# Kernel optimization log

Measured on AMD Instinct MI355X. Metric: run time of the kernel, lower is better.

## Reference

```python
import jax, jax.numpy as jnp
import numpy as np

B, GH, GW = 64, 14, 14
H = 512   # features_len == lstm hidden size == lstm_len
E = 512   # embedding_len
A = 512   # attention_len
V = 10000 # wordmap_len
MAXCAP = 50


def setup_inputs() -> dict:
    key = jax.random.key(0)
    ks = jax.random.split(key, 12)
    s = 0.02
    caplens = jax.random.randint(ks[2], (B, 1), 2, MAXCAP + 1, jnp.int32)
    caplens = caplens.at[0, 0].set(MAXCAP)  # ensure max(decode_lengths) == MAXCAP-1 (static T)
    return dict(
        image_features=jax.random.normal(ks[0], (B, GH, GW, H), jnp.float32),
        caps=jax.random.randint(ks[1], (B, MAXCAP), 0, V, jnp.int32),
        caplens=caplens,
        emb_table=jax.random.normal(ks[3], (V, E), jnp.float32) * s,
        W_ih=jax.random.normal(ks[4], (4 * H, E + H), jnp.float32) * s,
        W_hh=jax.random.normal(ks[5], (4 * H, H), jnp.float32) * s,
        b_ih=jnp.zeros((4 * H,), jnp.float32),
        b_hh=jnp.zeros((4 * H,), jnp.float32),
        W_enc=jax.random.normal(ks[6], (A, H), jnp.float32) * s,
        b_enc=jnp.zeros((A,), jnp.float32),
        W_dec=jax.random.normal(ks[7], (A, H), jnp.float32) * s,
        b_dec=jnp.zeros((A,), jnp.float32),
        W_full=jax.random.normal(ks[8], (1, A), jnp.float32) * s,
        b_full=jnp.zeros((1,), jnp.float32),
        W_score=jax.random.normal(ks[9], (V, H), jnp.float32) * s,
        b_score=jnp.zeros((V,), jnp.float32),
    )


def _forward(image_features, emb_table, W_ih, W_hh, b_ih, b_hh,
             W_enc, b_enc, W_dec, b_dec, W_full, b_full, W_score, b_score,
             caps, caplens):
    Bsz = image_features.shape[0]
    feats = image_features.reshape(Bsz, -1, image_features.shape[-1])  # (B, P, H)
    cl = caplens[:, 0]
    sort_ind = jnp.argsort(-cl)                      # descending sort by caption length
    cl = cl[sort_ind]
    feats = feats[sort_ind]
    caps_s = caps[sort_ind]
    decode_lengths = cl - 1
    T = caps.shape[1] - 1                            # static; setup guarantees max(decode_lengths)==T
    emb = emb_table[caps_s]                          # (B, MAXCAP, E)
    enc_att = jnp.einsum('bph,ah->bpa', feats, W_enc) + b_enc  # precomputed encoder attention proj
    mask = jnp.arange(T)[None, :] < decode_lengths[:, None]    # (B, T): row active at step t

    h0 = jnp.zeros((Bsz, feats.shape[-1]), feats.dtype)
    c0 = jnp.zeros_like(h0)

    def step(carry, xs):
        h, c = carry
        emb_t, m_t = xs                              # (B,E), (B,)
        # attention (show-attend-tell style)
        att2 = h @ W_dec.T + b_dec                   # (B, A)
        e = jnp.einsum('bpa,a->bp', jax.nn.relu(enc_att + att2[:, None, :]), W_full[0]) + b_full[0]
        alpha = jax.nn.softmax(e, axis=-1)           # (B, P)
        ctx = jnp.einsum('bp,bph->bh', alpha, feats) # (B, H)
        # LSTMCell
        x = jnp.concatenate([emb_t, ctx], axis=1)    # (B, E+H)
        gates = x @ W_ih.T + b_ih + h @ W_hh.T + b_hh
        i, f, g, o = jnp.split(gates, 4, axis=1)
        c_new = jax.nn.sigmoid(f) * c + jax.nn.sigmoid(i) * jnp.tanh(g)
        h_new = jax.nn.sigmoid(o) * jnp.tanh(c_new)
        score = h_new @ W_score.T + b_score          # (B, V)
        m = m_t[:, None]
        # rows past their decode length keep stale state and write zeros (matches :k slicing)
        h = jnp.where(m, h_new, h)
        c = jnp.where(m, c_new, c)
        return (h, c), (jnp.where(m, score, jnp.zeros((), score.dtype)),
                        jnp.where(m, alpha, jnp.zeros((), alpha.dtype)))

    (_, _), (scores, weights) = jax.lax.scan(
        step, (h0, c0), (emb[:, :T, :].transpose(1, 0, 2), mask.T))
    scores = scores.transpose(1, 0, 2)   # (B, T, V)
    weights = weights.transpose(1, 0, 2) # (B, T, P)
    return scores, caps_s, decode_lengths, weights, sort_ind


def reference(image_features, caps, caplens, emb_table, W_ih, W_hh, b_ih, b_hh,
              W_enc, b_enc, W_dec, b_dec, W_full, b_full, W_score, b_score):
    return _forward(image_features, emb_table, W_ih, W_hh, b_ih, b_hh,
                    W_enc, b_enc, W_dec, b_dec, W_full, b_full, W_score, b_score,
                    caps, caplens)
```

## Files before the change

kernel.cpp:

```cpp
#include <hip/hip_runtime.h>
#include <math.h>


#define WS_SORT   0
#define WS_DL     64
#define WS_NB     128
#define WS_ROWOFF 192
#define WS_CAPS   256
#define WS_RMAP   3456
#define WS_H      6592
#define WS_C      39360
#define WS_ATT2   72128
#define WS_E      104896
#define WS_Z      117696
#define WS_CTXP   117952
#define WS_PG     249024
#define WS_HALL   2346176
#define WS_ENC    3951808

#define OUT_SCORES 0
#define OUT_CAPS   31360000
#define OUT_DL     31363200
#define OUT_W      31363264
#define OUT_SORT   31977920

#define KC  32
#define LST 68
#define LSW 196

__device__ __forceinline__ float sigm(float x) { return 1.f / (1.f + expf(-x)); }

__device__ __forceinline__ float4 f4add(float4 a, float4 b) {
  return make_float4(a.x + b.x, a.y + b.y, a.z + b.z, a.w + b.w);
}

__device__ __forceinline__ int swz128(int m) { return (m >> 3) * 12 + (m & 7); }

__device__ __forceinline__ void gemm_acc(const float* __restrict__ As, const float* __restrict__ Bs,
                                         float acc[8][8], int tx, int ty) {
#pragma unroll 8
  for (int kk = 0; kk < KC; ++kk) {
    const float4* ar = (const float4*)(As + kk * LST + tx * 8);
    const float4* br = (const float4*)(Bs + kk * LST + ty * 8);
    float4 a0 = ar[0], a1 = ar[1];
    float4 b0 = br[0], b1 = br[1];
    float av[8] = {a0.x, a0.y, a0.z, a0.w, a1.x, a1.y, a1.z, a1.w};
    float bv[8] = {b0.x, b0.y, b0.z, b0.w, b1.x, b1.y, b1.z, b1.w};
#pragma unroll
    for (int i = 0; i < 8; ++i)
#pragma unroll
      for (int j = 0; j < 8; ++j)
        acc[i][j] = fmaf(av[i], bv[j], acc[i][j]);
  }
}

__device__ __forceinline__ void load_tile_strided(const float* __restrict__ src, int row0, int ld, int k0,
                                                  float* __restrict__ dst, int tid, int nrows_valid) {
#pragma unroll
  for (int i = 0; i < 8; ++i) {
    int lin = tid + 64 * i;
    int m = lin >> 3, kf = lin & 7;
    float4 v = make_float4(0.f, 0.f, 0.f, 0.f);
    if (m < nrows_valid) v = *(const float4*)(src + (long)(row0 + m) * ld + k0 + kf * 4);
    dst[(kf * 4 + 0) * LST + m] = v.x;
    dst[(kf * 4 + 1) * LST + m] = v.y;
    dst[(kf * 4 + 2) * LST + m] = v.z;
    dst[(kf * 4 + 3) * LST + m] = v.w;
  }
}

__device__ __forceinline__ void load_tile_gather(const float* __restrict__ src, const int* __restrict__ bases,
                                                 int k0, float* __restrict__ dst, int tid) {
#pragma unroll
  for (int i = 0; i < 8; ++i) {
    int lin = tid + 64 * i;
    int m = lin >> 3, kf = lin & 7;
    float4 v = *(const float4*)(src + bases[m] + k0 + kf * 4);
    dst[(kf * 4 + 0) * LST + m] = v.x;
    dst[(kf * 4 + 1) * LST + m] = v.y;
    dst[(kf * 4 + 2) * LST + m] = v.z;
    dst[(kf * 4 + 3) * LST + m] = v.w;
  }
}

__device__ __forceinline__ void stage128_strided(const float* __restrict__ src, int row0, int ld, int k0,
                                                 float* __restrict__ dst, int tid, int nrows_valid) {
#pragma unroll
  for (int i = 0; i < 2; ++i) {
    int lin = tid + 256 * i;
    int m = lin >> 2, kf = lin & 3;
    float4 v = make_float4(0.f, 0.f, 0.f, 0.f);
    if (m < nrows_valid) v = *(const float4*)(src + (long)(row0 + m) * ld + k0 + kf * 4);
    int mc = swz128(m);
    dst[(kf * 4 + 0) * LSW + mc] = v.x;
    dst[(kf * 4 + 1) * LSW + mc] = v.y;
    dst[(kf * 4 + 2) * LSW + mc] = v.z;
    dst[(kf * 4 + 3) * LSW + mc] = v.w;
  }
}

__device__ __forceinline__ void stage128_gather(const float* __restrict__ src, const int* __restrict__ bases,
                                                int k0, float* __restrict__ dst, int tid) {
#pragma unroll
  for (int i = 0; i < 2; ++i) {
    int lin = tid + 256 * i;
    int m = lin >> 2, kf = lin & 3;
    float4 v = *(const float4*)(src + bases[m] + k0 + kf * 4);
    int mc = swz128(m);
    dst[(kf * 4 + 0) * LSW + mc] = v.x;
    dst[(kf * 4 + 1) * LSW + mc] = v.y;
    dst[(kf * 4 + 2) * LSW + mc] = v.z;
    dst[(kf * 4 + 3) * LSW + mc] = v.w;
  }
}

__device__ __forceinline__ void gemm_acc128(const float* __restrict__ As, const float* __restrict__ Bs,
                                            float acc[8][8], int tx, int ty) {
#pragma unroll
  for (int kk = 0; kk < 16; ++kk) {
    const float4* ar = (const float4*)(As + kk * LSW + tx * 12);
    const float4* br = (const float4*)(Bs + kk * LSW + ty * 12);
    float4 a0 = ar[0], a1 = ar[1];
    float4 b0 = br[0], b1 = br[1];
    float av[8] = {a0.x, a0.y, a0.z, a0.w, a1.x, a1.y, a1.z, a1.w};
    float bv[8] = {b0.x, b0.y, b0.z, b0.w, b1.x, b1.y, b1.z, b1.w};
#pragma unroll
    for (int i = 0; i < 8; ++i)
#pragma unroll
      for (int j = 0; j < 8; ++j)
        acc[i][j] = fmaf(av[i], bv[j], acc[i][j]);
  }
}

__global__ __launch_bounds__(64) void setup_kernel(const int* __restrict__ caps, const int* __restrict__ caplens,
                                                   float* __restrict__ ws, float* __restrict__ out) {
  __shared__ int cl_s[64], so_s[64], dl_s[64], nb_s[49], ro_s[50];
  int i = threadIdx.x;
  cl_s[i] = caplens[i];
  __syncthreads();
  int cli = cl_s[i];
  int r = 0;
  for (int j = 0; j < 64; ++j) {
    int clj = cl_s[j];
    r += (clj > cli) || (clj == cli && j < i);
  }
  so_s[r] = i;
  dl_s[r] = cli - 1;
  __syncthreads();
  int* iws = (int*)ws;
  iws[WS_SORT + i] = so_s[i];
  iws[WS_DL + i] = dl_s[i];
  out[OUT_SORT + i] = (float)so_s[i];
  out[OUT_DL + i] = (float)dl_s[i];
  if (i < 49) {
    int n = 0;
    for (int b = 0; b < 64; ++b) n += (dl_s[b] > i);
    iws[WS_NB + i] = n;
    nb_s[i] = n;
  }
  __syncthreads();
  if (i == 0) {
    int acc = 0;
    for (int t = 0; t < 49; ++t) { ro_s[t] = acc; acc += nb_s[t]; }
    ro_s[49] = acc;
    iws[WS_NB + 49] = acc;
  }
  __syncthreads();
  if (i < 50) iws[WS_ROWOFF + i] = ro_s[i];
  int R = ro_s[49];
  for (int rr = i; rr < 3136; rr += 64) {
    int val = 0;
    if (rr < R) {
      int t = 0;
      while (t < 48 && ro_s[t + 1] <= rr) ++t;
      val = t * 64 + (rr - ro_s[t]);
    }
    iws[WS_RMAP + rr] = val;
  }
  for (int j = i; j < 3200; j += 64) {
    int k = j / 50, jj = j - k * 50;
    int cv = caps[so_s[k] * 50 + jj];
    iws[WS_CAPS + j] = cv;
    out[OUT_CAPS + j] = (float)cv;
  }
}

__global__ void zero_init_kernel(float* __restrict__ out, float* __restrict__ ws, const float* __restrict__ b_dec) {
  const float4 z = make_float4(0.f, 0.f, 0.f, 0.f);
  float4* out4 = (float4*)out;
  float4* ws4 = (float4*)ws;
  const float4* bd4 = (const float4*)b_dec;
  for (long idx = (long)blockIdx.x * 256 + threadIdx.x; idx < 8018240L; idx += (long)gridDim.x * 256) {
    if (idx < 7840000L) {
      out4[idx] = z;
    } else if (idx < 7993664L) {
      out4[7840816L + (idx - 7840000L)] = z;
    } else if (idx < 8010048L) {
      ws4[1648L + (idx - 7993664L)] = z;
    } else {
      long j = idx - 8010048L;
      ws4[18032L + j] = bd4[j & 127];
    }
  }
}

__global__ __launch_bounds__(256) void encatt_kernel(const float* __restrict__ image, const float* __restrict__ W_enc,
                                                     const float* __restrict__ b_enc, float* __restrict__ ws) {
  __shared__ __align__(16) float As[16 * LSW];
  __shared__ __align__(16) float Bs[16 * LSW];
  __shared__ int rb[128];
  int tid = threadIdx.x;
  const int* iws = (const int*)ws;
  int mt = blockIdx.x, nt = blockIdx.y;
  if (tid < 128) {
    int r = mt * 128 + tid;
    int b = r / 196;
    int p = r - b * 196;
    rb[tid] = iws[WS_SORT + b] * 100352 + p * 512;
  }
  float acc[8][8] = {};
  for (int ch = 0; ch < 32; ++ch) {
    __syncthreads();
    stage128_gather(image, rb, ch * 16, As, tid);
    stage128_strided(W_enc, nt * 128, 512, ch * 16, Bs, tid, 128);
    __syncthreads();
    gemm_acc128(As, Bs, acc, tid & 15, tid >> 4);
  }
  int tx = tid & 15, ty = tid >> 4;
  int r0 = mt * 128 + tx * 8;
  int n0 = nt * 128 + ty * 8;
#pragma unroll
  for (int i = 0; i < 8; ++i) {
    float* cp = ws + WS_ENC + (long)(r0 + i) * 512 + n0;
    *(float4*)(cp)     = make_float4(acc[i][0] + b_enc[n0],     acc[i][1] + b_enc[n0 + 1],
                                     acc[i][2] + b_enc[n0 + 2], acc[i][3] + b_enc[n0 + 3]);
    *(float4*)(cp + 4) = make_float4(acc[i][4] + b_enc[n0 + 4], acc[i][5] + b_enc[n0 + 5],
                                     acc[i][6] + b_enc[n0 + 6], acc[i][7] + b_enc[n0 + 7]);
  }
}

__global__ __launch_bounds__(512) void ectx_kernel(float* __restrict__ ws, const float* __restrict__ image,
                                                   const float* __restrict__ W_full, const float* __restrict__ b_full,
                                                   int t) {
  const int* iws = (const int*)ws;
  int b = blockIdx.x;
  if (b >= iws[WS_NB + t]) return;
  int pg = blockIdx.y;
  __shared__ float e_s[64];
  __shared__ __align__(16) float ctxp_s[2048];
  int tid = threadIdx.x;
  int w = tid >> 6, lane = tid & 63;

  float4 at0 = *(const float4*)(ws + WS_ATT2 + b * 512 + lane * 4);
  float4 at1 = *(const float4*)(ws + WS_ATT2 + b * 512 + 256 + lane * 4);
  float4 wf0 = *(const float4*)(W_full + lane * 4);
  float4 wf1 = *(const float4*)(W_full + 256 + lane * 4);
  float bf0 = b_full[0];

  for (int idx = w; idx < 49; idx += 8) {
    const float* er = ws + WS_ENC + (long)(b * 196 + pg * 49 + idx) * 512;
    float4 e0 = *(const float4*)(er + lane * 4);
    float4 e1 = *(const float4*)(er + 256 + lane * 4);
    float acc = fmaxf(e0.x + at0.x, 0.f) * wf0.x + fmaxf(e0.y + at0.y, 0.f) * wf0.y +
                fmaxf(e0.z + at0.z, 0.f) * wf0.z + fmaxf(e0.w + at0.w, 0.f) * wf0.w +
                fmaxf(e1.x + at1.x, 0.f) * wf1.x + fmaxf(e1.y + at1.y, 0.f) * wf1.y +
                fmaxf(e1.z + at1.z, 0.f) * wf1.z + fmaxf(e1.w + at1.w, 0.f) * wf1.w;
#pragma unroll
    for (int off = 32; off; off >>= 1) acc += __shfl_down(acc, off);
    if (lane == 0) e_s[idx] = expf(acc + bf0);
  }
  __syncthreads();
  if (tid < 49) ws[WS_E + b * 200 + pg * 49 + tid] = e_s[tid];
  if (tid < 64) {
    float zv = (tid < 49) ? e_s[tid] : 0.f;
#pragma unroll
    for (int off = 32; off; off >>= 1) zv += __shfl_down(zv, off);
    if (tid == 0) ws[WS_Z + pg * 64 + b] = zv;
  }
  long sb = (long)iws[WS_SORT + b] * 100352;
  int rg = tid >> 7, l1 = tid & 127;
  float4 a = make_float4(0.f, 0.f, 0.f, 0.f);
  for (int idx = rg; idx < 49; idx += 4) {
    float al = e_s[idx];
    float4 v = *(const float4*)(image + sb + (long)(pg * 49 + idx) * 512 + l1 * 4);
    a.x = fmaf(al, v.x, a.x); a.y = fmaf(al, v.y, a.y);
    a.z = fmaf(al, v.z, a.z); a.w = fmaf(al, v.w, a.w);
  }
  *(float4*)(ctxp_s + rg * 512 + l1 * 4) = a;
  __syncthreads();
  if (tid < 128) {
    float4 v0 = *(const float4*)(ctxp_s + tid * 4);
    float4 v1 = *(const float4*)(ctxp_s + 512 + tid * 4);
    float4 v2 = *(const float4*)(ctxp_s + 1024 + tid * 4);
    float4 v3 = *(const float4*)(ctxp_s + 1536 + tid * 4);
    *(float4*)(ws + WS_CTXP + pg * 32768 + b * 512 + tid * 4) =
        make_float4(v0.x + v1.x + v2.x + v3.x, v0.y + v1.y + v2.y + v3.y,
                    v0.z + v1.z + v2.z + v3.z, v0.w + v1.w + v2.w + v3.w);
  }
}

__global__ __launch_bounds__(64) void gates_kernel(float* __restrict__ ws, const float* __restrict__ emb,
                                                   const float* __restrict__ W_ih, const float* __restrict__ W_hh,
                                                   int t) {
  __shared__ __align__(16) float As[KC * LST];
  __shared__ __align__(16) float Bs[KC * LST];
  __shared__ int rbe[64];
  __shared__ float rcpz_s[64];
  int tid = threadIdx.x;
  int nt = blockIdx.x;
  int ks = blockIdx.y;
  int* iws = (int*)ws;
  rbe[tid] = iws[WS_CAPS + tid * 50 + t] * 512;
  {
    float zz = ws[WS_Z + tid] + ws[WS_Z + 64 + tid] + ws[WS_Z + 128 + tid] + ws[WS_Z + 192 + tid];
    rcpz_s[tid] = 1.f / zz;
  }
  float acc[8][8] = {};
  for (int ch = 0; ch < 3; ++ch) {
    int k0 = ks * 96 + ch * 32;
    __syncthreads();
    if (k0 < 512) {
      load_tile_gather(emb, rbe, k0, As, tid);
    } else if (k0 < 1024) {
      int kc = k0 - 512;
#pragma unroll
      for (int i = 0; i < 8; ++i) {
        int lin = tid + 64 * i;
        int m = lin >> 3, kf = lin & 7;
        const float* base = ws + WS_CTXP + m * 512 + kc + kf * 4;
        float4 v0 = *(const float4*)(base);
        float4 v1 = *(const float4*)(base + 32768);
        float4 v2 = *(const float4*)(base + 65536);
        float4 v3 = *(const float4*)(base + 98304);
        float rz = rcpz_s[m];
        As[(kf * 4 + 0) * LST + m] = (v0.x + v1.x + v2.x + v3.x) * rz;
        As[(kf * 4 + 1) * LST + m] = (v0.y + v1.y + v2.y + v3.y) * rz;
        As[(kf * 4 + 2) * LST + m] = (v0.z + v1.z + v2.z + v3.z) * rz;
        As[(kf * 4 + 3) * LST + m] = (v0.w + v1.w + v2.w + v3.w) * rz;
      }
    } else {
      load_tile_strided(ws + WS_H, 0, 512, k0 - 1024, As, tid, 64);
    }
    if (k0 < 1024) load_tile_strided(W_ih, nt * 64, 1024, k0, Bs, tid, 64);
    else           load_tile_strided(W_hh, nt * 64, 512, k0 - 1024, Bs, tid, 64);
    __syncthreads();
    gemm_acc(As, Bs, acc, tid & 7, tid >> 3);
  }
  int tx = tid & 7, ty = tid >> 3;
  float* pg = ws + WS_PG + ks * 131072;
  int j0 = nt * 64 + ty * 8;
#pragma unroll
  for (int i = 0; i < 8; ++i) {
    int b = tx * 8 + i;
    float* cp = pg + b * 2048 + j0;
    *(float4*)(cp)     = make_float4(acc[i][0], acc[i][1], acc[i][2], acc[i][3]);
    *(float4*)(cp + 4) = make_float4(acc[i][4], acc[i][5], acc[i][6], acc[i][7]);
  }
}

__global__ __launch_bounds__(512) void lstm_att2_kernel(float* __restrict__ ws, const float* __restrict__ b_ih,
                                                        const float* __restrict__ b_hh, const float* __restrict__ W_dec,
                                                        const float* __restrict__ b_dec, float* __restrict__ out, int t) {
  const int* iws = (const int*)ws;
  int b = blockIdx.x;
  if (b >= iws[WS_NB + t]) return;
  int as = blockIdx.y;
  int hh = threadIdx.x;
  __shared__ __align__(16) float g[2048];
  __shared__ float h_s[512], red[512];
  const float4* bi4 = (const float4*)b_ih;
  const float4* bh4 = (const float4*)b_hh;
  float4 A = f4add(bi4[hh], bh4[hh]);
  const float* pgb = ws + WS_PG + b * 2048;
#pragma unroll
  for (int ks = 0; ks < 16; ++ks) {
    A = f4add(A, *(const float4*)(pgb + (long)ks * 131072 + hh * 4));
  }
  *(float4*)(g + hh * 4) = A;
  __syncthreads();
  float gi = g[hh], gf = g[512 + hh], gg = g[1024 + hh], go = g[1536 + hh];
  float c = ws[WS_C + b * 512 + hh];
  float cn = sigm(gf) * c + sigm(gi) * tanhf(gg);
  float hn = sigm(go) * tanhf(cn);
  h_s[hh] = hn;
  if (as == 0) {
    ws[WS_C + b * 512 + hh] = cn;
    ws[WS_H + b * 512 + hh] = hn;
    ws[WS_HALL + (long)(iws[WS_ROWOFF + t] + b) * 512 + hh] = hn;
  }
  if (hh < 49) {
    float zz = ws[WS_Z + b] + ws[WS_Z + 64 + b] + ws[WS_Z + 128 + b] + ws[WS_Z + 192 + b];
    int p = as * 49 + hh;
    out[OUT_W + (long)(b * 49 + t) * 196 + p] = ws[WS_E + b * 200 + p] / zz;
  }
  __syncthreads();
  int a = as * 128 + (hh >> 2);
  int part = hh & 3;
  const float* wd = W_dec + (long)a * 512 + part * 128;
  const float* hp = h_s + part * 128;
  float s = 0.f;
#pragma unroll 8
  for (int j = 0; j < 32; ++j) {
    float4 wv = *(const float4*)(wd + 4 * j);
    s = fmaf(hp[4 * j], wv.x, s);
    s = fmaf(hp[4 * j + 1], wv.y, s);
    s = fmaf(hp[4 * j + 2], wv.z, s);
    s = fmaf(hp[4 * j + 3], wv.w, s);
  }
  red[hh] = s;
  __syncthreads();
  if (part == 0) {
    float v = red[hh] + red[hh + 1] + red[hh + 2] + red[hh + 3] + b_dec[a];
    ws[WS_ATT2 + b * 512 + a] = v;
  }
}

__global__ __launch_bounds__(256) void score_kernel(const float* __restrict__ ws, const float* __restrict__ W_score,
                                                    const float* __restrict__ b_score, float* __restrict__ out) {
  __shared__ __align__(16) float As[16 * LSW];
  __shared__ __align__(16) float Bs[16 * LSW];
  const int* iws = (const int*)ws;
  int mt = blockIdx.x, nt = blockIdx.y;
  int R = iws[WS_NB + 49];
  if (mt * 128 >= R) return;
  int tid = threadIdx.x;
  int mvalid = R - mt * 128; if (mvalid > 128) mvalid = 128;
  int nvalid = 10000 - nt * 128; if (nvalid > 128) nvalid = 128;
  float acc[8][8] = {};
  for (int ch = 0; ch < 32; ++ch) {
    __syncthreads();
    stage128_strided(ws + WS_HALL, mt * 128, 512, ch * 16, As, tid, mvalid);
    stage128_strided(W_score, nt * 128, 512, ch * 16, Bs, tid, nvalid);
    __syncthreads();
    gemm_acc128(As, Bs, acc, tid & 15, tid >> 4);
  }
  int tx = tid & 15, ty = tid >> 4;
  int n0 = nt * 128 + ty * 8;
#pragma unroll
  for (int i = 0; i < 8; ++i) {
    int r = mt * 128 + tx * 8 + i;
    if (r >= R) continue;
    int tb = iws[WS_RMAP + r];
    int bb = tb & 63, tt = tb >> 6;
    float* cp = out + (long)bb * 490000 + tt * 10000 + n0;
    if (n0 + 4 <= 10000)
      *(float4*)(cp)     = make_float4(acc[i][0] + b_score[n0],     acc[i][1] + b_score[n0 + 1],
                                       acc[i][2] + b_score[n0 + 2], acc[i][3] + b_score[n0 + 3]);
    if (n0 + 8 <= 10000)
      *(float4*)(cp + 4) = make_float4(acc[i][4] + b_score[n0 + 4], acc[i][5] + b_score[n0 + 5],
                                       acc[i][6] + b_score[n0 + 6], acc[i][7] + b_score[n0 + 7]);
  }
}

extern "C" void kernel_launch(void* const* d_in, const int* in_sizes, int n_in,
                              void* d_out, int out_size, void* d_ws, size_t ws_size,
                              hipStream_t stream) {
  const float* image   = (const float*)d_in[0];
  const int*   caps    = (const int*)d_in[1];
  const int*   caplens = (const int*)d_in[2];
  const float* emb     = (const float*)d_in[3];
  const float* W_ih    = (const float*)d_in[4];
  const float* W_hh    = (const float*)d_in[5];
  const float* b_ih    = (const float*)d_in[6];
  const float* b_hh    = (const float*)d_in[7];
  const float* W_enc   = (const float*)d_in[8];
  const float* b_enc   = (const float*)d_in[9];
  const float* W_dec   = (const float*)d_in[10];
  const float* b_dec   = (const float*)d_in[11];
  const float* W_full  = (const float*)d_in[12];
  const float* b_full  = (const float*)d_in[13];
  const float* W_score = (const float*)d_in[14];
  const float* b_score = (const float*)d_in[15];
  float* out = (float*)d_out;
  float* ws  = (float*)d_ws;

  setup_kernel<<<1, 64, 0, stream>>>(caps, caplens, ws, out);
  zero_init_kernel<<<2048, 256, 0, stream>>>(out, ws, b_dec);
  encatt_kernel<<<dim3(98, 4), 256, 0, stream>>>(image, W_enc, b_enc, ws);
  for (int t = 0; t < 49; ++t) {
    ectx_kernel<<<dim3(64, 4), 512, 0, stream>>>(ws, image, W_full, b_full, t);
    gates_kernel<<<dim3(32, 16), 64, 0, stream>>>(ws, emb, W_ih, W_hh, t);
    lstm_att2_kernel<<<dim3(64, 4), 512, 0, stream>>>(ws, b_ih, b_hh, W_dec, b_dec, out, t);
  }
  score_kernel<<<dim3(25, 79), 256, 0, stream>>>(ws, W_score, b_score, out);
}
```

Baseline: 2.616 ms.

## Retile per-step gates GEMM into 256-thread blocks with single-stage full-K load

The per-step gates GEMM changes from 64-thread blocks computing a 64x64 tile over three 32-wide K chunks to 256-thread blocks computing a 64x128 tile. Each block stages its whole 96-wide K slice of activations and weights into shared memory at once, then does a single synchronised FMA loop. Four waves per block and fewer barriers are meant to improve latency hiding and cut sync overhead for this small launch-bound kernel. In exchange the grid has half as many blocks, each using more shared memory (about 77 KB), which may lower occupancy.

```diff
diff --git a/kernel.cpp b/kernel.cpp
--- a/kernel.cpp
+++ b/kernel.cpp
@@ -24,8 +24,6 @@
 #define OUT_W      31363264
 #define OUT_SORT   31977920
 
-#define KC  32
-#define LST 68
 #define LSW 196
 
 __device__ __forceinline__ float sigm(float x) { return 1.f / (1.f + expf(-x)); }
@@ -35,53 +33,6 @@
 }
 
 __device__ __forceinline__ int swz128(int m) { return (m >> 3) * 12 + (m & 7); }
-
-__device__ __forceinline__ void gemm_acc(const float* __restrict__ As, const float* __restrict__ Bs,
-                                         float acc[8][8], int tx, int ty) {
-#pragma unroll 8
-  for (int kk = 0; kk < KC; ++kk) {
-    const float4* ar = (const float4*)(As + kk * LST + tx * 8);
-    const float4* br = (const float4*)(Bs + kk * LST + ty * 8);
-    float4 a0 = ar[0], a1 = ar[1];
-    float4 b0 = br[0], b1 = br[1];
-    float av[8] = {a0.x, a0.y, a0.z, a0.w, a1.x, a1.y, a1.z, a1.w};
-    float bv[8] = {b0.x, b0.y, b0.z, b0.w, b1.x, b1.y, b1.z, b1.w};
-#pragma unroll
-    for (int i = 0; i < 8; ++i)
-#pragma unroll
-      for (int j = 0; j < 8; ++j)
-        acc[i][j] = fmaf(av[i], bv[j], acc[i][j]);
-  }
-}
-
-__device__ __forceinline__ void load_tile_strided(const float* __restrict__ src, int row0, int ld, int k0,
-                                                  float* __restrict__ dst, int tid, int nrows_valid) {
-#pragma unroll
-  for (int i = 0; i < 8; ++i) {
-    int lin = tid + 64 * i;
-    int m = lin >> 3, kf = lin & 7;
-    float4 v = make_float4(0.f, 0.f, 0.f, 0.f);
-    if (m < nrows_valid) v = *(const float4*)(src + (long)(row0 + m) * ld + k0 + kf * 4);
-    dst[(kf * 4 + 0) * LST + m] = v.x;
-    dst[(kf * 4 + 1) * LST + m] = v.y;
-    dst[(kf * 4 + 2) * LST + m] = v.z;
-    dst[(kf * 4 + 3) * LST + m] = v.w;
-  }
-}
-
-__device__ __forceinline__ void load_tile_gather(const float* __restrict__ src, const int* __restrict__ bases,
-                                                 int k0, float* __restrict__ dst, int tid) {
-#pragma unroll
-  for (int i = 0; i < 8; ++i) {
-    int lin = tid + 64 * i;
-    int m = lin >> 3, kf = lin & 7;
-    float4 v = *(const float4*)(src + bases[m] + k0 + kf * 4);
-    dst[(kf * 4 + 0) * LST + m] = v.x;
-    dst[(kf * 4 + 1) * LST + m] = v.y;
-    dst[(kf * 4 + 2) * LST + m] = v.z;
-    dst[(kf * 4 + 3) * LST + m] = v.w;
-  }
-}
 
 __device__ __forceinline__ void stage128_strided(const float* __restrict__ src, int row0, int ld, int k0,
                                                  float* __restrict__ dst, int tid, int nrows_valid) {
@@ -299,62 +250,82 @@
   }
 }
 
-__global__ __launch_bounds__(64) void gates_kernel(float* __restrict__ ws, const float* __restrict__ emb,
-                                                   const float* __restrict__ W_ih, const float* __restrict__ W_hh,
-                                                   int t) {
-  __shared__ __align__(16) float As[KC * LST];
-  __shared__ __align__(16) float Bs[KC * LST];
+__global__ __launch_bounds__(256) void gates_kernel(float* __restrict__ ws, const float* __restrict__ emb,
+                                                    const float* __restrict__ W_ih, const float* __restrict__ W_hh,
+                                                    int t) {
+  __shared__ __align__(16) float As[96 * 68];
+  __shared__ __align__(16) float Bs[96 * 132];
   __shared__ int rbe[64];
   __shared__ float rcpz_s[64];
   int tid = threadIdx.x;
   int nt = blockIdx.x;
   int ks = blockIdx.y;
-  int* iws = (int*)ws;
-  rbe[tid] = iws[WS_CAPS + tid * 50 + t] * 512;
-  {
+  const int* iws = (const int*)ws;
+  if (tid < 64) {
+    rbe[tid] = iws[WS_CAPS + tid * 50 + t] * 512;
     float zz = ws[WS_Z + tid] + ws[WS_Z + 64 + tid] + ws[WS_Z + 128 + tid] + ws[WS_Z + 192 + tid];
     rcpz_s[tid] = 1.f / zz;
   }
-  float acc[8][8] = {};
-  for (int ch = 0; ch < 3; ++ch) {
-    int k0 = ks * 96 + ch * 32;
-    __syncthreads();
-    if (k0 < 512) {
-      load_tile_gather(emb, rbe, k0, As, tid);
-    } else if (k0 < 1024) {
-      int kc = k0 - 512;
-#pragma unroll
-      for (int i = 0; i < 8; ++i) {
-        int lin = tid + 64 * i;
-        int m = lin >> 3, kf = lin & 7;
-        const float* base = ws + WS_CTXP + m * 512 + kc + kf * 4;
-        float4 v0 = *(const float4*)(base);
-        float4 v1 = *(const float4*)(base + 32768);
-        float4 v2 = *(const float4*)(base + 65536);
-        float4 v3 = *(const float4*)(base + 98304);
-        float rz = rcpz_s[m];
-        As[(kf * 4 + 0) * LST + m] = (v0.x + v1.x + v2.x + v3.x) * rz;
-        As[(kf * 4 + 1) * LST + m] = (v0.y + v1.y + v2.y + v3.y) * rz;
-        As[(kf * 4 + 2) * LST + m] = (v0.z + v1.z + v2.z + v3.z) * rz;
-        As[(kf * 4 + 3) * LST + m] = (v0.w + v1.w + v2.w + v3.w) * rz;
-      }
+  __syncthreads();
+  int k0 = ks * 96;
+#pragma unroll
+  for (int i = 0; i < 6; ++i) {
+    int c = tid + 256 * i;
+    int m = c / 24, kf = c - m * 24;
+    int k = k0 + kf * 4;
+    float4 v;
+    if (k < 512) {
+      v = *(const float4*)(emb + (long)rbe[m] + k);
+    } else if (k < 1024) {
+      const float* base = ws + WS_CTXP + m * 512 + (k - 512);
+      float4 v0 = *(const float4*)(base);
+      float4 v1 = *(const float4*)(base + 32768);
+      float4 v2 = *(const float4*)(base + 65536);
+      float4 v3 = *(const float4*)(base + 98304);
+      float rz = rcpz_s[m];
+      v = make_float4((v0.x + v1.x + v2.x + v3.x) * rz, (v0.y + v1.y + v2.y + v3.y) * rz,
+                      (v0.z + v1.z + v2.z + v3.z) * rz, (v0.w + v1.w + v2.w + v3.w) * rz);
     } else {
-      load_tile_strided(ws + WS_H, 0, 512, k0 - 1024, As, tid, 64);
+      v = *(const float4*)(ws + WS_H + m * 512 + (k - 1024));
     }
-    if (k0 < 1024) load_tile_strided(W_ih, nt * 64, 1024, k0, Bs, tid, 64);
-    else           load_tile_strided(W_hh, nt * 64, 512, k0 - 1024, Bs, tid, 64);
-    __syncthreads();
-    gemm_acc(As, Bs, acc, tid & 7, tid >> 3);
-  }
-  int tx = tid & 7, ty = tid >> 3;
+    float* da = As + (kf * 4) * 68 + m;
+    da[0] = v.x; da[68] = v.y; da[136] = v.z; da[204] = v.w;
+  }
+#pragma unroll
+  for (int i = 0; i < 12; ++i) {
+    int c = tid + 256 * i;
+    int m = c / 24, kf = c - m * 24;
+    int k = k0 + kf * 4;
+    int row = nt * 128 + m;
+    const float* srcB = (k < 1024) ? (W_ih + (long)row * 1024 + k)
+                                   : (W_hh + (long)row * 512 + (k - 1024));
+    float4 v = *(const float4*)srcB;
+    float* db = Bs + (kf * 4) * 132 + m;
+    db[0] = v.x; db[132] = v.y; db[264] = v.z; db[396] = v.w;
+  }
+  __syncthreads();
+  int w = tid >> 6, lane = tid & 63;
+  int tx = lane & 7, ty = lane >> 3;
+  float acc[8][4] = {};
+#pragma unroll 4
+  for (int kk = 0; kk < 96; ++kk) {
+    const float4* ar = (const float4*)(As + kk * 68 + tx * 8);
+    float4 a0 = ar[0], a1 = ar[1];
+    float4 bv = *(const float4*)(Bs + kk * 132 + w * 32 + ty * 4);
+    float av[8] = {a0.x, a0.y, a0.z, a0.w, a1.x, a1.y, a1.z, a1.w};
+#pragma unroll
+    for (int i = 0; i < 8; ++i) {
+      acc[i][0] = fmaf(av[i], bv.x, acc[i][0]);
+      acc[i][1] = fmaf(av[i], bv.y, acc[i][1]);
+      acc[i][2] = fmaf(av[i], bv.z, acc[i][2]);
+      acc[i][3] = fmaf(av[i], bv.w, acc[i][3]);
+    }
+  }
   float* pg = ws + WS_PG + ks * 131072;
-  int j0 = nt * 64 + ty * 8;
+  int j0 = nt * 128 + w * 32 + ty * 4;
 #pragma unroll
   for (int i = 0; i < 8; ++i) {
-    int b = tx * 8 + i;
-    float* cp = pg + b * 2048 + j0;
-    *(float4*)(cp)     = make_float4(acc[i][0], acc[i][1], acc[i][2], acc[i][3]);
-    *(float4*)(cp + 4) = make_float4(acc[i][4], acc[i][5], acc[i][6], acc[i][7]);
+    *(float4*)(pg + (tx * 8 + i) * 2048 + j0) = make_float4(acc[i][0], acc[i][1], acc[i][2], acc[i][3]);
   }
 }
 
@@ -479,7 +450,7 @@
   encatt_kernel<<<dim3(98, 4), 256, 0, stream>>>(image, W_enc, b_enc, ws);
   for (int t = 0; t < 49; ++t) {
     ectx_kernel<<<dim3(64, 4), 512, 0, stream>>>(ws, image, W_full, b_full, t);
-    gates_kernel<<<dim3(32, 16), 64, 0, stream>>>(ws, emb, W_ih, W_hh, t);
+    gates_kernel<<<dim3(16, 16), 256, 0, stream>>>(ws, emb, W_ih, W_hh, t);
     lstm_att2_kernel<<<dim3(64, 4), 512, 0, stream>>>(ws, b_ih, b_hh, W_dec, b_dec, out, t);
   }
   score_kernel<<<dim3(25, 79), 256, 0, stream>>>(ws, W_score, b_score, out);
```

Result: no change. 2.625 ms (+0.3%).
